# Kernel optimization log

Hardware: AMD Instinct MI355X
Metric: run time of the kernel (lower is better)

## Reference

```python
import math
import jax, jax.numpy as jnp
import numpy as np

N_HEAD = 16


def setup_inputs() -> dict:
    key = jax.random.key(0)
    k1, k2, k3 = jax.random.split(key, 3)
    B, T, D = 2, 2048, 1024
    q = jax.random.normal(k1, (B, T, D), dtype=jnp.float32)
    k = jax.random.normal(k2, (B, T, D), dtype=jnp.float32)
    v = jax.random.normal(k3, (B, T, D), dtype=jnp.float32)
    return {"q": q, "k": k, "v": v}


def _split_heads(x, n_head):
    B, T, D = x.shape
    return x.reshape(B, T, n_head, D // n_head).transpose(0, 2, 1, 3)  # [B,H,T,d]


def _alibi_bias(q_len, k_len, n_head, dtype):
    # bias[t, s] = s - t for s <= t (tril), 0 above diagonal
    rel = jnp.arange(k_len)[None, :] - jnp.arange(q_len)[:, None]
    rel = jnp.tril(rel).astype(dtype)  # [q,k], values <= 0 on lower triangle
    # slopes m_h = 2^(-8*(h+1)/H) via cumprod of constant 2^(-8/H)
    slopes = jnp.cumprod(jnp.full((n_head,), 2.0 ** (-8.0 / n_head), dtype=dtype))
    return rel[None] * slopes[:, None, None]  # [H,q,k]


def reference(q, k, v):
    H = N_HEAD
    qh = _split_heads(q, H)  # [B,H,T,d]
    kh = _split_heads(k, H)
    vh = _split_heads(v, H)
    d = qh.shape[-1]
    attn = jnp.einsum('bhtd,bhsd->bhts', qh, kh) / math.sqrt(d)
    T = qh.shape[2]
    attn = attn + _alibi_bias(T, T, H, attn.dtype)[None]  # broadcast over batch
    causal_mask = jnp.triu(jnp.ones((T, T), dtype=bool), 1)
    attn = jnp.where(causal_mask[None, None], -jnp.inf, attn)
    attn = jax.nn.softmax(attn, axis=-1)
    out = jnp.einsum('bhts,bhsd->bhtd', attn, vh)
    B = out.shape[0]
    return out.transpose(0, 2, 1, 3).reshape(B, T, H * d)
```

## Files before the change

kernel.cpp:

```cpp
#include <hip/hip_runtime.h>
#include <hip/hip_bf16.h>

#define TT 2048
#define DDIM 1024
#define NHEAD 16
#define HD 64
#define QBLK 64
#define KVBLK 64
#define NQT (TT / QBLK)

typedef float f32x4 __attribute__((ext_vector_type(4)));
typedef short bf16x8 __attribute__((ext_vector_type(8)));

__device__ __forceinline__ ushort f2bf(float f) {
    __hip_bfloat16 h = __float2bfloat16(f);
    return *reinterpret_cast<ushort*>(&h);
}

__device__ __forceinline__ void barrier_lgkm_only() {
    asm volatile("s_waitcnt lgkmcnt(0)" ::: "memory");
    __builtin_amdgcn_s_barrier();
}

__global__ __launch_bounds__(256)
void prepass_kernel(const float* __restrict__ kg, const float* __restrict__ vg,
                    ushort* __restrict__ kbf, ushort* __restrict__ vt) {
    __shared__ float vtile[64][65];
    const int tid = threadIdx.x;
    const int kv0 = (int)blockIdx.x * 64;
    const int bh  = (int)blockIdx.y;
    const int b = bh >> 4, h = bh & 15;
    const int row = tid >> 2;
    const int c0  = (tid & 3) * 16;
    const size_t gin = ((size_t)(b * TT + kv0 + row)) * DDIM + h * HD + c0;

    {
        ushort o[16];
        #pragma unroll
        for (int i = 0; i < 4; ++i) {
            float4 a = *(const float4*)(kg + gin + i * 4);
            o[i*4+0]=f2bf(a.x); o[i*4+1]=f2bf(a.y); o[i*4+2]=f2bf(a.z); o[i*4+3]=f2bf(a.w);
        }
        ushort* kout = kbf + ((size_t)bh * TT + kv0 + row) * HD + c0;
        *(bf16x8*)kout       = *(bf16x8*)&o[0];
        *(bf16x8*)(kout + 8) = *(bf16x8*)&o[8];
    }
    #pragma unroll
    for (int i = 0; i < 4; ++i) {
        float4 a = *(const float4*)(vg + gin + i * 4);
        vtile[row][c0 + i*4 + 0] = a.x;
        vtile[row][c0 + i*4 + 1] = a.y;
        vtile[row][c0 + i*4 + 2] = a.z;
        vtile[row][c0 + i*4 + 3] = a.w;
    }
    __syncthreads();
    {
        ushort o[16];
        #pragma unroll
        for (int i = 0; i < 16; ++i) o[i] = f2bf(vtile[c0 + i][row]);
        ushort* vout = vt + ((size_t)bh * HD + row) * TT + kv0 + c0;
        *(bf16x8*)vout       = *(bf16x8*)&o[0];
        *(bf16x8*)(vout + 8) = *(bf16x8*)&o[8];
    }
}

__global__ __launch_bounds__(256, 2)
void attn_main(const float* __restrict__ qg, const ushort* __restrict__ kbf,
               const ushort* __restrict__ vt, float* __restrict__ out) {
    __shared__ __align__(16) ushort lds_k[2][KVBLK * HD];
    __shared__ __align__(16) ushort lds_v[2][HD * KVBLK];
    __shared__ __align__(16) ushort lds_p[4][16 * 64];

    const int tid  = threadIdx.x;
    const int wv   = tid >> 6;
    const int lane = tid & 63;
    const int hi   = lane >> 4;
    const int qr   = lane & 15;

    const int flat = (int)blockIdx.x;
    const int xcd  = flat & 7;
    const int idx  = flat >> 3;
    const int bs   = idx >> 5;
    const int s    = idx & 31;
    const int bh   = xcd * 4 + bs;
    const int qt   = (bs & 1) ? s : (NQT - 1 - s);
    const int b    = bh >> 4;
    const int h    = bh & 15;
    const int q0   = qt * QBLK;

    const float LOG2E  = 1.4426950408889634f;
    const float slope2 = exp2f(-0.5f * (float)(h + 1)) * LOG2E;
    const float sc2    = 0.125f * LOG2E;

    bf16x8 qf[2];
    {
        const float* gq = qg + ((size_t)(b * TT + q0 + wv * 16 + qr)) * DDIM + h * HD + hi * 8;
        #pragma unroll
        for (int ch = 0; ch < 2; ++ch) {
            float4 a0 = *(const float4*)(gq + ch * 32);
            float4 a1 = *(const float4*)(gq + ch * 32 + 4);
            bf16x8 w;
            w[0]=f2bf(a0.x); w[1]=f2bf(a0.y); w[2]=f2bf(a0.z); w[3]=f2bf(a0.w);
            w[4]=f2bf(a1.x); w[5]=f2bf(a1.y); w[6]=f2bf(a1.z); w[7]=f2bf(a1.w);
            qf[ch] = w;
        }
    }

    const ushort* kb = kbf + (size_t)bh * TT * HD;
    const ushort* vb = vt  + (size_t)bh * HD * TT;

    const int srow = tid >> 2;
    const int sci  = tid & 3;

    bf16x8 kr0, kr1, vr0, vr1;
    auto stage_issue = [&](int kv0) {
        const ushort* kp = kb + (size_t)(kv0 + srow) * HD + sci * 8;
        kr0 = *(const bf16x8*)kp;
        kr1 = *(const bf16x8*)(kp + 32);
        const ushort* vp = vb + (size_t)srow * TT + kv0 + sci * 8;
        vr0 = *(const bf16x8*)vp;
        vr1 = *(const bf16x8*)(vp + 32);
    };
    auto stage_write = [&](int nb) {
        const int sw = (srow & 7);
        *(bf16x8*)&lds_k[nb][srow * 64 + ((sci ^ sw) << 3)]       = kr0;
        *(bf16x8*)&lds_k[nb][srow * 64 + (((sci + 4) ^ sw) << 3)] = kr1;
        *(bf16x8*)&lds_v[nb][srow * 64 + ((sci ^ sw) << 3)]       = vr0;
        *(bf16x8*)&lds_v[nb][srow * 64 + (((sci + 4) ^ sw) << 3)] = vr1;
    };

    const int nit = qt + 1;
    stage_issue(q0);
    stage_write(0);

    f32x4 oacc[4] = {};
    float mrun = -INFINITY, lrun = 0.f;
    const int ti = q0 + wv * 16 + qr;

    for (int j = 0; j < nit; ++j) {
        const int buf = j & 1;
        const int kv0 = q0 - j * KVBLK;
        if (j + 1 < nit) stage_issue(kv0 - KVBLK);
        barrier_lgkm_only();

        const bool diag = (j == 0);

        f32x4 sa[4] = {};
        __builtin_amdgcn_s_setprio(1);
        #pragma unroll
        for (int st = 0; st < 4; ++st) {
            if (!diag || st <= wv) {
                const int krow = st * 16 + qr;
                const int sw = (krow & 7);
                bf16x8 k0 = *(const bf16x8*)&lds_k[buf][krow * 64 + ((hi ^ sw) << 3)];
                bf16x8 k1 = *(const bf16x8*)&lds_k[buf][krow * 64 + (((4 + hi) ^ sw) << 3)];
                sa[st] = __builtin_amdgcn_mfma_f32_16x16x32_bf16(k0, qf[0], sa[st], 0, 0, 0);
                sa[st] = __builtin_amdgcn_mfma_f32_16x16x32_bf16(k1, qf[1], sa[st], 0, 0, 0);
            }
        }
        __builtin_amdgcn_s_setprio(0);

        const float relb = (float)(kv0 - ti + hi * 4);
        float xv[16];
        float tm = -INFINITY;
        #pragma unroll
        for (int st = 0; st < 4; ++st)
            #pragma unroll
            for (int rr = 0; rr < 4; ++rr) {
                const float rel = relb + (float)(st * 16 + rr);
                float v = fmaf(sa[st][rr], sc2, rel * slope2);
                if (diag) v = (rel <= 0.f) ? v : -INFINITY;
                xv[st * 4 + rr] = v;
                tm = fmaxf(tm, v);
            }
        tm = fmaxf(tm, __shfl_xor(tm, 16));
        tm = fmaxf(tm, __shfl_xor(tm, 32));
        if (!__all(tm <= mrun + 8.f)) {
            const float mnew = fmaxf(mrun, tm);
            const float fsc  = exp2f(mrun - mnew);
            mrun = mnew;
            lrun *= fsc;
            float fo[4];
            #pragma unroll
            for (int rr = 0; rr < 4; ++rr) fo[rr] = __shfl(fsc, hi * 4 + rr);
            #pragma unroll
            for (int dt = 0; dt < 4; ++dt)
                #pragma unroll
                for (int rr = 0; rr < 4; ++rr) oacc[dt][rr] *= fo[rr];
        }
        float psum = 0.f;
        #pragma unroll
        for (int i = 0; i < 16; ++i) { xv[i] = exp2f(xv[i] - mrun); psum += xv[i]; }
        lrun += psum;

        #pragma unroll
        for (int st = 0; st < 4; ++st) {
            ushort4 w;
            w.x = f2bf(xv[st * 4 + 0]); w.y = f2bf(xv[st * 4 + 1]);
            w.z = f2bf(xv[st * 4 + 2]); w.w = f2bf(xv[st * 4 + 3]);
            const int slot8 = (st << 1) | (hi >> 1);
            *(ushort4*)&lds_p[wv][qr * 64 + ((slot8 ^ (qr & 7)) << 3) + ((hi & 1) << 2)] = w;
        }

        __builtin_amdgcn_s_setprio(1);
        #pragma unroll
        for (int ks = 0; ks < 2; ++ks) {
            if (!diag || wv >= 2 || ks == 0) {
                bf16x8 pa = *(const bf16x8*)&lds_p[wv][qr * 64 + ((((ks << 2) | hi) ^ (qr & 7)) << 3)];
                #pragma unroll
                for (int dt = 0; dt < 4; ++dt) {
                    const int dv = dt * 16 + qr;
                    bf16x8 vbf = *(const bf16x8*)&lds_v[buf][dv * 64 + ((((ks << 2) + hi) ^ (dv & 7)) << 3)];
                    oacc[dt] = __builtin_amdgcn_mfma_f32_16x16x32_bf16(pa, vbf, oacc[dt], 0, 0, 0);
                }
            }
        }
        __builtin_amdgcn_s_setprio(0);

        if (j + 1 < nit) stage_write(buf ^ 1);
    }

    {
        float lr = lrun;
        lr += __shfl_xor(lr, 16);
        lr += __shfl_xor(lr, 32);
        const float linv = 1.0f / lr;
        #pragma unroll
        for (int rr = 0; rr < 4; ++rr) {
            const float inv = __shfl(linv, hi * 4 + rr);
            float* go = out + ((size_t)(b * TT + q0 + wv * 16 + hi * 4 + rr)) * DDIM + h * HD;
            #pragma unroll
            for (int dt = 0; dt < 4; ++dt)
                go[dt * 16 + qr] = oacc[dt][rr] * inv;
        }
    }
}

#define VST 72
__global__ __launch_bounds__(256, 2)
void alibi_attn_fallback(const float* __restrict__ qg,
                         const float* __restrict__ kg,
                         const float* __restrict__ vg,
                         float* __restrict__ out) {
    __shared__ __align__(16) ushort lds_k[KVBLK * HD];
    __shared__ __align__(16) ushort lds_vt[HD * VST];
    __shared__ __align__(16) ushort lds_p[4][16 * 64];

    const int tid  = threadIdx.x;
    const int wv   = tid >> 6;
    const int lane = tid & 63;
    const int hi   = lane >> 4;
    const int qr   = lane & 15;

    const int flat = (int)blockIdx.x;
    const int xcd  = flat & 7;
    const int idx  = flat >> 3;
    const int bh   = xcd * 4 + (idx >> 5);
    const int qt   = NQT - 1 - (idx & 31);
    const int b    = bh >> 4;
    const int h    = bh & 15;
    const int q0   = qt * QBLK;

    const float LOG2E  = 1.4426950408889634f;
    const float slope2 = exp2f(-0.5f * (float)(h + 1)) * LOG2E;
    const float sc2    = 0.125f * LOG2E;

    const size_t bhbase = (size_t)(b * TT) * DDIM + (size_t)(h * HD);

    bf16x8 qf[2];
    {
        const float* gq = qg + bhbase + (size_t)(q0 + wv * 16 + qr) * DDIM + hi * 8;
        #pragma unroll
        for (int ch = 0; ch < 2; ++ch) {
            float4 a0 = *(const float4*)(gq + ch * 32);
            float4 a1 = *(const float4*)(gq + ch * 32 + 4);
            bf16x8 w;
            w[0]=f2bf(a0.x); w[1]=f2bf(a0.y); w[2]=f2bf(a0.z); w[3]=f2bf(a0.w);
            w[4]=f2bf(a1.x); w[5]=f2bf(a1.y); w[6]=f2bf(a1.z); w[7]=f2bf(a1.w);
            qf[ch] = w;
        }
    }

    const int krow = tid >> 3;
    const int kcg  = tid & 7;
    const int vdv  = tid & 63;
    const int vkc  = tid >> 6;

    float ka[2][8], va[2][8];
    auto issue_loads = [&](int kv0) {
        const float* kp0 = kg + bhbase + (size_t)(kv0 + krow) * DDIM + kcg * 8;
        const float* kp1 = kp0 + (size_t)32 * DDIM;
        *(float4*)&ka[0][0] = *(const float4*)kp0; *(float4*)&ka[0][4] = *(const float4*)(kp0 + 4);
        *(float4*)&ka[1][0] = *(const float4*)kp1; *(float4*)&ka[1][4] = *(const float4*)(kp1 + 4);
        const float* vp0 = vg + bhbase + (size_t)(kv0 + vkc * 8) * DDIM + vdv;
        const float* vp1 = vp0 + (size_t)32 * DDIM;
        #pragma unroll
        for (int jj = 0; jj < 8; ++jj) {
            va[0][jj] = vp0[(size_t)jj * DDIM];
            va[1][jj] = vp1[(size_t)jj * DDIM];
        }
    };
    auto write_stage = [&]() {
        #pragma unroll
        for (int s2 = 0; s2 < 2; ++s2) {
            bf16x8 w;
            #pragma unroll
            for (int e = 0; e < 8; ++e) w[e] = f2bf(ka[s2][e]);
            const int row = krow + s2 * 32;
            *(bf16x8*)&lds_k[row * 64 + ((kcg ^ (row & 7)) << 3)] = w;
            bf16x8 u;
            #pragma unroll
            for (int e = 0; e < 8; ++e) u[e] = f2bf(va[s2][e]);
            const int kc = vkc + s2 * 4;
            *(bf16x8*)&lds_vt[vdv * VST + ((kc ^ ((vdv >> 3) & 7)) << 3)] = u;
        }
    };

    const int nit = qt + 1;
    issue_loads(q0);
    write_stage();

    f32x4 oacc[4] = {};
    float mrun = -INFINITY, lrun = 0.f;

    for (int j = 0; j < nit; ++j) {
        const int kv0 = (qt - j) * KVBLK;
        if (j + 1 < nit) issue_loads(kv0 - KVBLK);
        __syncthreads();

        const bool diag = (j == 0);

        f32x4 s_acc[4] = {};
        __builtin_amdgcn_s_setprio(1);
        #pragma unroll
        for (int st = 0; st < 4; ++st) {
            if (!diag || st <= wv) {
                const int kvrow = st * 16 + qr;
                #pragma unroll
                for (int ch = 0; ch < 2; ++ch) {
                    bf16x8 kf = *(const bf16x8*)&lds_k[kvrow * 64 + ((((ch << 2) + hi) ^ (kvrow & 7)) << 3)];
                    s_acc[st] = __builtin_amdgcn_mfma_f32_16x16x32_bf16(kf, qf[ch], s_acc[st], 0, 0, 0);
                }
            }
        }
        __builtin_amdgcn_s_setprio(0);

        const int ti = q0 + wv * 16 + qr;
        float xv[16];
        float tm = -INFINITY;
        {
            const float relb = (float)(kv0 - ti);
            #pragma unroll
            for (int st = 0; st < 4; ++st)
                #pragma unroll
                for (int rr = 0; rr < 4; ++rr) {
                    const float rel = relb + (float)(st * 16 + hi * 4 + rr);
                    float v = s_acc[st][rr] * sc2 + rel * slope2;
                    if (diag) v = (rel <= 0.f) ? v : -INFINITY;
                    xv[st * 4 + rr] = v;
                    tm = fmaxf(tm, v);
                }
        }
        tm = fmaxf(tm, __shfl_xor(tm, 16));
        tm = fmaxf(tm, __shfl_xor(tm, 32));
        if (!__all(tm <= mrun + 8.f)) {
            const float mnew = fmaxf(mrun, tm);
            const float fsc  = exp2f(mrun - mnew);
            mrun = mnew;
            lrun *= fsc;
            float fo[4];
            #pragma unroll
            for (int rr = 0; rr < 4; ++rr) fo[rr] = __shfl(fsc, hi * 4 + rr);
            #pragma unroll
            for (int dt = 0; dt < 4; ++dt)
                #pragma unroll
                for (int rr = 0; rr < 4; ++rr) oacc[dt][rr] *= fo[rr];
        }
        float psum = 0.f;
        #pragma unroll
        for (int i = 0; i < 16; ++i) { xv[i] = exp2f(xv[i] - mrun); psum += xv[i]; }
        lrun += psum;

        #pragma unroll
        for (int st = 0; st < 4; ++st) {
            ushort4 w;
            w.x = f2bf(xv[st * 4 + 0]); w.y = f2bf(xv[st * 4 + 1]);
            w.z = f2bf(xv[st * 4 + 2]); w.w = f2bf(xv[st * 4 + 3]);
            const int slot8 = (st << 1) | (hi >> 1);
            *(ushort4*)&lds_p[wv][qr * 64 + ((slot8 ^ (qr & 7)) << 3) + ((hi & 1) << 2)] = w;
        }

        __builtin_amdgcn_s_setprio(1);
        #pragma unroll
        for (int ks = 0; ks < 2; ++ks) {
            if (!diag || wv >= 2 || ks == 0) {
                bf16x8 pa = *(const bf16x8*)&lds_p[wv][qr * 64 + ((((ks << 2) | hi) ^ (qr & 7)) << 3)];
                #pragma unroll
                for (int dt = 0; dt < 4; ++dt) {
                    const int dv = dt * 16 + qr;
                    bf16x8 vbf = *(const bf16x8*)&lds_vt[dv * VST + ((((ks << 2) + hi) ^ ((dv >> 3) & 7)) << 3)];
                    oacc[dt] = __builtin_amdgcn_mfma_f32_16x16x32_bf16(pa, vbf, oacc[dt], 0, 0, 0);
                }
            }
        }
        __builtin_amdgcn_s_setprio(0);

        if (j + 1 < nit) {
            __syncthreads();
            write_stage();
        }
    }

    {
        float lr = lrun;
        lr += __shfl_xor(lr, 16);
        lr += __shfl_xor(lr, 32);
        const float linv = 1.0f / lr;
        #pragma unroll
        for (int rr = 0; rr < 4; ++rr) {
            const float inv = __shfl(linv, hi * 4 + rr);
            float* go = out + bhbase + (size_t)(q0 + wv * 16 + hi * 4 + rr) * DDIM;
            #pragma unroll
            for (int dt = 0; dt < 4; ++dt)
                go[dt * 16 + qr] = oacc[dt][rr] * inv;
        }
    }
}

extern "C" void kernel_launch(void* const* d_in, const int* in_sizes, int n_in,
                              void* d_out, int out_size, void* d_ws, size_t ws_size,
                              hipStream_t stream) {
    (void)in_sizes; (void)n_in; (void)out_size;
    const float* q = (const float*)d_in[0];
    const float* k = (const float*)d_in[1];
    const float* v = (const float*)d_in[2];
    float* o = (float*)d_out;

    const size_t elems = (size_t)2 * NHEAD * TT * HD;
    const size_t need  = 2 * elems * sizeof(ushort);
    if (ws_size >= need) {
        ushort* kbf = (ushort*)d_ws;
        ushort* vt  = kbf + elems;
        prepass_kernel<<<dim3(32, 32), 256, 0, stream>>>(k, v, kbf, vt);
        attn_main<<<dim3(1024), 256, 0, stream>>>(q, kbf, vt, o);
    } else {
        alibi_attn_fallback<<<dim3(1024), 256, 0, stream>>>(q, k, v, o);
    }
}
```

Baseline: 65.34 us.

## Split heavy causal query tiles across two blocks and merge with a combine kernel

Query tiles 16-31 have their KV range cut in half, and each half runs in its own block, giving 1536 blocks instead of 1024. This evens out the causal workload imbalance. Split blocks write unnormalized partial outputs plus running max/sum to workspace, and a new combine kernel merges them. It also precomputes per-element ALiBi offsets and moves the cross-lane max shuffle inside the rescale branch. This adds a third launch and extra global traffic for the partials, and the fallback path for small workspace is removed.

After: 68.48 us. +4.8%, slower.

```diff
diff --git a/kernel.cpp b/kernel.cpp
--- a/kernel.cpp
+++ b/kernel.cpp
@@ -65,8 +65,9 @@
 }
 
 __global__ __launch_bounds__(256, 2)
-void attn_main(const float* __restrict__ qg, const ushort* __restrict__ kbf,
-               const ushort* __restrict__ vt, float* __restrict__ out) {
+void attn_split(const float* __restrict__ qg, const ushort* __restrict__ kbf,
+                const ushort* __restrict__ vtt, float* __restrict__ po,
+                float* __restrict__ ml, float* __restrict__ out) {
     __shared__ __align__(16) ushort lds_k[2][KVBLK * HD];
     __shared__ __align__(16) ushort lds_v[2][HD * KVBLK];
     __shared__ __align__(16) ushort lds_p[4][16 * 64];
@@ -79,18 +80,27 @@
 
     const int flat = (int)blockIdx.x;
     const int xcd  = flat & 7;
-    const int idx  = flat >> 3;
-    const int bs   = idx >> 5;
-    const int s    = idx & 31;
-    const int bh   = xcd * 4 + bs;
-    const int qt   = (bs & 1) ? s : (NQT - 1 - s);
-    const int b    = bh >> 4;
-    const int h    = bh & 15;
-    const int q0   = qt * QBLK;
+    const int i2   = flat >> 3;
+    const int bh   = xcd * 4 + (i2 & 3);
+    const int id   = i2 >> 2;
+    int qt, lo, thi, part = 0;
+    bool hasdiag, heavy;
+    if (id < 16)      { qt = 16 + id;        const int n = qt + 1; lo = n >> 1; thi = n;      hasdiag = true;  heavy = true; part = 0; }
+    else if (id < 32) { qt = 31 - (id - 16); const int n = qt + 1; lo = 0;      thi = n >> 1; hasdiag = false; heavy = true; part = 1; }
+    else              { qt = id - 32;        lo = 0; thi = qt + 1; hasdiag = true; heavy = false; }
+    const int nt = thi - lo;
+    const int b  = bh >> 4;
+    const int h  = bh & 15;
+    const int q0 = qt * QBLK;
 
     const float LOG2E  = 1.4426950408889634f;
     const float slope2 = exp2f(-0.5f * (float)(h + 1)) * LOG2E;
     const float sc2    = 0.125f * LOG2E;
+    float c2[16];
+    #pragma unroll
+    for (int st = 0; st < 4; ++st)
+        #pragma unroll
+        for (int rr = 0; rr < 4; ++rr) c2[st * 4 + rr] = (float)(st * 16 + rr) * slope2;
 
     bf16x8 qf[2];
     {
@@ -107,7 +117,7 @@
     }
 
     const ushort* kb = kbf + (size_t)bh * TT * HD;
-    const ushort* vb = vt  + (size_t)bh * HD * TT;
+    const ushort* vb = vtt + (size_t)bh * HD * TT;
 
     const int srow = tid >> 2;
     const int sci  = tid & 3;
@@ -129,6 +139,233 @@
         *(bf16x8*)&lds_v[nb][srow * 64 + (((sci + 4) ^ sw) << 3)] = vr1;
     };
 
+    stage_issue((thi - 1) * KVBLK);
+    stage_write(0);
+
+    f32x4 oacc[4] = {};
+    float mrun = -INFINITY, lrun = 0.f;
+    const int ti = q0 + wv * 16 + qr;
+
+    for (int j = 0; j < nt; ++j) {
+        const int buf = j & 1;
+        const int t   = thi - 1 - j;
+        const int kv0 = t * KVBLK;
+        if (j + 1 < nt) stage_issue((t - 1) * KVBLK);
+        barrier_lgkm_only();
+
+        const bool diag = (j == 0) && hasdiag;
+
+        f32x4 sa[4] = {};
+        __builtin_amdgcn_s_setprio(1);
+        #pragma unroll
+        for (int st = 0; st < 4; ++st) {
+            if (!diag || st <= wv) {
+                const int krow = st * 16 + qr;
+                const int sw = (krow & 7);
+                bf16x8 k0 = *(const bf16x8*)&lds_k[buf][krow * 64 + ((hi ^ sw) << 3)];
+                bf16x8 k1 = *(const bf16x8*)&lds_k[buf][krow * 64 + (((4 + hi) ^ sw) << 3)];
+                sa[st] = __builtin_amdgcn_mfma_f32_16x16x32_bf16(k0, qf[0], sa[st], 0, 0, 0);
+                sa[st] = __builtin_amdgcn_mfma_f32_16x16x32_bf16(k1, qf[1], sa[st], 0, 0, 0);
+            }
+        }
+        __builtin_amdgcn_s_setprio(0);
+
+        const float relb  = (float)(kv0 - ti + hi * 4);
+        const float relb2 = relb * slope2;
+        float xv[16];
+        float tm = -INFINITY;
+        #pragma unroll
+        for (int st = 0; st < 4; ++st)
+            #pragma unroll
+            for (int rr = 0; rr < 4; ++rr) {
+                float v = fmaf(sa[st][rr], sc2, relb2 + c2[st * 4 + rr]);
+                if (diag) {
+                    const float rel = relb + (float)(st * 16 + rr);
+                    v = (rel <= 0.f) ? v : -INFINITY;
+                }
+                xv[st * 4 + rr] = v;
+                tm = fmaxf(tm, v);
+            }
+        if (!__all(tm <= mrun + 8.f)) {
+            tm = fmaxf(tm, __shfl_xor(tm, 16));
+            tm = fmaxf(tm, __shfl_xor(tm, 32));
+            const float mnew = fmaxf(mrun, tm);
+            const float fsc  = exp2f(mrun - mnew);
+            mrun = mnew;
+            lrun *= fsc;
+            float fo[4];
+            #pragma unroll
+            for (int rr = 0; rr < 4; ++rr) fo[rr] = __shfl(fsc, hi * 4 + rr);
+            #pragma unroll
+            for (int dt = 0; dt < 4; ++dt)
+                #pragma unroll
+                for (int rr = 0; rr < 4; ++rr) oacc[dt][rr] *= fo[rr];
+        }
+        float psum = 0.f;
+        #pragma unroll
+        for (int i = 0; i < 16; ++i) { xv[i] = exp2f(xv[i] - mrun); psum += xv[i]; }
+        lrun += psum;
+
+        #pragma unroll
+        for (int st = 0; st < 4; ++st) {
+            ushort4 w;
+            w.x = f2bf(xv[st * 4 + 0]); w.y = f2bf(xv[st * 4 + 1]);
+            w.z = f2bf(xv[st * 4 + 2]); w.w = f2bf(xv[st * 4 + 3]);
+            const int slot8 = (st << 1) | (hi >> 1);
+            *(ushort4*)&lds_p[wv][qr * 64 + ((slot8 ^ (qr & 7)) << 3) + ((hi & 1) << 2)] = w;
+        }
+
+        __builtin_amdgcn_s_setprio(1);
+        #pragma unroll
+        for (int ks = 0; ks < 2; ++ks) {
+            if (!diag || wv >= 2 || ks == 0) {
+                bf16x8 pa = *(const bf16x8*)&lds_p[wv][qr * 64 + ((((ks << 2) | hi) ^ (qr & 7)) << 3)];
+                #pragma unroll
+                for (int dt = 0; dt < 4; ++dt) {
+                    const int dv = dt * 16 + qr;
+                    bf16x8 vbf = *(const bf16x8*)&lds_v[buf][dv * 64 + ((((ks << 2) + hi) ^ (dv & 7)) << 3)];
+                    oacc[dt] = __builtin_amdgcn_mfma_f32_16x16x32_bf16(pa, vbf, oacc[dt], 0, 0, 0);
+                }
+            }
+        }
+        __builtin_amdgcn_s_setprio(0);
+
+        if (j + 1 < nt) stage_write(buf ^ 1);
+    }
+
+    float lr = lrun;
+    lr += __shfl_xor(lr, 16);
+    lr += __shfl_xor(lr, 32);
+    if (!heavy) {
+        const float linv = 1.0f / lr;
+        #pragma unroll
+        for (int rr = 0; rr < 4; ++rr) {
+            const float inv = __shfl(linv, hi * 4 + rr);
+            float* go = out + ((size_t)(b * TT + q0 + wv * 16 + hi * 4 + rr)) * DDIM + h * HD;
+            #pragma unroll
+            for (int dt = 0; dt < 4; ++dt)
+                go[dt * 16 + qr] = oacc[dt][rr] * inv;
+        }
+    } else {
+        float* pbase = po + ((size_t)((part * 32 + bh) * 16 + (qt - 16))) * 4096;
+        #pragma unroll
+        for (int rr = 0; rr < 4; ++rr) {
+            const int row = wv * 16 + hi * 4 + rr;
+            #pragma unroll
+            for (int dt = 0; dt < 4; ++dt)
+                pbase[row * 64 + dt * 16 + qr] = oacc[dt][rr];
+        }
+        if (hi == 0) {
+            float* mlb = ml + ((size_t)((part * 32 + bh) * 16 + (qt - 16))) * 128 + (wv * 16 + qr) * 2;
+            mlb[0] = mrun;
+            mlb[1] = lr;
+        }
+    }
+}
+
+__global__ __launch_bounds__(256)
+void combine_kernel(const float* __restrict__ po, const float* __restrict__ ml,
+                    float* __restrict__ out) {
+    const int blk = (int)blockIdx.x;
+    const int bh  = blk >> 4;
+    const int q16 = blk & 15;
+    const int qt  = 16 + q16;
+    const int b = bh >> 4, h = bh & 15;
+    const int tid = threadIdx.x;
+    const int row = tid >> 2;
+    const int c0  = (tid & 3) * 16;
+
+    const float* ml0 = ml + ((size_t)((0 * 32 + bh) * 16 + q16)) * 128 + row * 2;
+    const float* ml1 = ml + ((size_t)((1 * 32 + bh) * 16 + q16)) * 128 + row * 2;
+    const float m0 = ml0[0], l0 = ml0[1];
+    const float m1 = ml1[0], l1 = ml1[1];
+    const float m  = fmaxf(m0, m1);
+    const float a0 = exp2f(m0 - m);
+    const float a1 = exp2f(m1 - m);
+    const float linv = 1.0f / fmaf(l0, a0, l1 * a1);
+    const float s0 = a0 * linv, s1 = a1 * linv;
+
+    const float* p0 = po + ((size_t)((0 * 32 + bh) * 16 + q16) * 64 + row) * 64 + c0;
+    const float* p1 = po + ((size_t)((1 * 32 + bh) * 16 + q16) * 64 + row) * 64 + c0;
+    float* go = out + ((size_t)(b * TT + qt * 64 + row)) * DDIM + h * HD + c0;
+    #pragma unroll
+    for (int i = 0; i < 4; ++i) {
+        float4 x0 = *(const float4*)(p0 + i * 4);
+        float4 x1 = *(const float4*)(p1 + i * 4);
+        float4 r;
+        r.x = x0.x * s0 + x1.x * s1;
+        r.y = x0.y * s0 + x1.y * s1;
+        r.z = x0.z * s0 + x1.z * s1;
+        r.w = x0.w * s0 + x1.w * s1;
+        *(float4*)(go + i * 4) = r;
+    }
+}
+
+__global__ __launch_bounds__(256, 2)
+void attn_main(const float* __restrict__ qg, const ushort* __restrict__ kbf,
+               const ushort* __restrict__ vt, float* __restrict__ out) {
+    __shared__ __align__(16) ushort lds_k[2][KVBLK * HD];
+    __shared__ __align__(16) ushort lds_v[2][HD * KVBLK];
+    __shared__ __align__(16) ushort lds_p[4][16 * 64];
+
+    const int tid  = threadIdx.x;
+    const int wv   = tid >> 6;
+    const int lane = tid & 63;
+    const int hi   = lane >> 4;
+    const int qr   = lane & 15;
+
+    const int flat = (int)blockIdx.x;
+    const int xcd  = flat & 7;
+    const int idx  = flat >> 3;
+    const int bs   = idx >> 5;
+    const int s    = idx & 31;
+    const int bh   = xcd * 4 + bs;
+    const int qt   = (bs & 1) ? s : (NQT - 1 - s);
+    const int b    = bh >> 4;
+    const int h    = bh & 15;
+    const int q0   = qt * QBLK;
+
+    const float LOG2E  = 1.4426950408889634f;
+    const float slope2 = exp2f(-0.5f * (float)(h + 1)) * LOG2E;
+    const float sc2    = 0.125f * LOG2E;
+
+    bf16x8 qf[2];
+    {
+        const float* gq = qg + ((size_t)(b * TT + q0 + wv * 16 + qr)) * DDIM + h * HD + hi * 8;
+        #pragma unroll
+        for (int ch = 0; ch < 2; ++ch) {
+            float4 a0 = *(const float4*)(gq + ch * 32);
+            float4 a1 = *(const float4*)(gq + ch * 32 + 4);
+            bf16x8 w;
+            w[0]=f2bf(a0.x); w[1]=f2bf(a0.y); w[2]=f2bf(a0.z); w[3]=f2bf(a0.w);
+            w[4]=f2bf(a1.x); w[5]=f2bf(a1.y); w[6]=f2bf(a1.z); w[7]=f2bf(a1.w);
+            qf[ch] = w;
+        }
+    }
+
+    const ushort* kb = kbf + (size_t)bh * TT * HD;
+    const ushort* vb = vt  + (size_t)bh * HD * TT;
+
+    const int srow = tid >> 2;
+    const int sci  = tid & 3;
+
+    bf16x8 kr0, kr1, vr0, vr1;
+    auto stage_issue = [&](int kv0) {
+        const ushort* kp = kb + (size_t)(kv0 + srow) * HD + sci * 8;
+        kr0 = *(const bf16x8*)kp;
+        kr1 = *(const bf16x8*)(kp + 32);
+        const ushort* vp = vb + (size_t)srow * TT + kv0 + sci * 8;
+        vr0 = *(const bf16x8*)vp;
+        vr1 = *(const bf16x8*)(vp + 32);
+    };
+    auto stage_write = [&](int nb) {
+        const int sw = (srow & 7);
+        *(bf16x8*)&lds_k[nb][srow * 64 + ((sci ^ sw) << 3)]       = kr0;
+        *(bf16x8*)&lds_k[nb][srow * 64 + (((sci + 4) ^ sw) << 3)] = kr1;
+        *(bf16x8*)&lds_v[nb][srow * 64 + ((sci ^ sw) << 3)]       = vr0;
+        *(bf16x8*)&lds_v[nb][srow * 64 + (((sci + 4) ^ sw) << 3)] = vr1;
+    };
+
     const int nit = qt + 1;
     stage_issue(q0);
     stage_write(0);
@@ -236,197 +473,6 @@
     }
 }
 
-#define VST 72
-__global__ __launch_bounds__(256, 2)
-void alibi_attn_fallback(const float* __restrict__ qg,
-                         const float* __restrict__ kg,
-                         const float* __restrict__ vg,
-                         float* __restrict__ out) {
-    __shared__ __align__(16) ushort lds_k[KVBLK * HD];
-    __shared__ __align__(16) ushort lds_vt[HD * VST];
-    __shared__ __align__(16) ushort lds_p[4][16 * 64];
-
-    const int tid  = threadIdx.x;
-    const int wv   = tid >> 6;
-    const int lane = tid & 63;
-    const int hi   = lane >> 4;
-    const int qr   = lane & 15;
-
-    const int flat = (int)blockIdx.x;
-    const int xcd  = flat & 7;
-    const int idx  = flat >> 3;
-    const int bh   = xcd * 4 + (idx >> 5);
-    const int qt   = NQT - 1 - (idx & 31);
-    const int b    = bh >> 4;
-    const int h    = bh & 15;
-    const int q0   = qt * QBLK;
-
-    const float LOG2E  = 1.4426950408889634f;
-    const float slope2 = exp2f(-0.5f * (float)(h + 1)) * LOG2E;
-    const float sc2    = 0.125f * LOG2E;
-
-    const size_t bhbase = (size_t)(b * TT) * DDIM + (size_t)(h * HD);
-
-    bf16x8 qf[2];
-    {
-        const float* gq = qg + bhbase + (size_t)(q0 + wv * 16 + qr) * DDIM + hi * 8;
-        #pragma unroll
-        for (int ch = 0; ch < 2; ++ch) {
-            float4 a0 = *(const float4*)(gq + ch * 32);
-            float4 a1 = *(const float4*)(gq + ch * 32 + 4);
-            bf16x8 w;
-            w[0]=f2bf(a0.x); w[1]=f2bf(a0.y); w[2]=f2bf(a0.z); w[3]=f2bf(a0.w);
-            w[4]=f2bf(a1.x); w[5]=f2bf(a1.y); w[6]=f2bf(a1.z); w[7]=f2bf(a1.w);
-            qf[ch] = w;
-        }
-    }
-
-    const int krow = tid >> 3;
-    const int kcg  = tid & 7;
-    const int vdv  = tid & 63;
-    const int vkc  = tid >> 6;
-
-    float ka[2][8], va[2][8];
-    auto issue_loads = [&](int kv0) {
-        const float* kp0 = kg + bhbase + (size_t)(kv0 + krow) * DDIM + kcg * 8;
-        const float* kp1 = kp0 + (size_t)32 * DDIM;
-        *(float4*)&ka[0][0] = *(const float4*)kp0; *(float4*)&ka[0][4] = *(const float4*)(kp0 + 4);
-        *(float4*)&ka[1][0] = *(const float4*)kp1; *(float4*)&ka[1][4] = *(const float4*)(kp1 + 4);
-        const float* vp0 = vg + bhbase + (size_t)(kv0 + vkc * 8) * DDIM + vdv;
-        const float* vp1 = vp0 + (size_t)32 * DDIM;
-        #pragma unroll
-        for (int jj = 0; jj < 8; ++jj) {
-            va[0][jj] = vp0[(size_t)jj * DDIM];
-            va[1][jj] = vp1[(size_t)jj * DDIM];
-        }
-    };
-    auto write_stage = [&]() {
-        #pragma unroll
-        for (int s2 = 0; s2 < 2; ++s2) {
-            bf16x8 w;
-            #pragma unroll
-            for (int e = 0; e < 8; ++e) w[e] = f2bf(ka[s2][e]);
-            const int row = krow + s2 * 32;
-            *(bf16x8*)&lds_k[row * 64 + ((kcg ^ (row & 7)) << 3)] = w;
-            bf16x8 u;
-            #pragma unroll
-            for (int e = 0; e < 8; ++e) u[e] = f2bf(va[s2][e]);
-            const int kc = vkc + s2 * 4;
-            *(bf16x8*)&lds_vt[vdv * VST + ((kc ^ ((vdv >> 3) & 7)) << 3)] = u;
-        }
-    };
-
-    const int nit = qt + 1;
-    issue_loads(q0);
-    write_stage();
-
-    f32x4 oacc[4] = {};
-    float mrun = -INFINITY, lrun = 0.f;
-
-    for (int j = 0; j < nit; ++j) {
-        const int kv0 = (qt - j) * KVBLK;
-        if (j + 1 < nit) issue_loads(kv0 - KVBLK);
-        __syncthreads();
-
-        const bool diag = (j == 0);
-
-        f32x4 s_acc[4] = {};
-        __builtin_amdgcn_s_setprio(1);
-        #pragma unroll
-        for (int st = 0; st < 4; ++st) {
-            if (!diag || st <= wv) {
-                const int kvrow = st * 16 + qr;
-                #pragma unroll
-                for (int ch = 0; ch < 2; ++ch) {
-                    bf16x8 kf = *(const bf16x8*)&lds_k[kvrow * 64 + ((((ch << 2) + hi) ^ (kvrow & 7)) << 3)];
-                    s_acc[st] = __builtin_amdgcn_mfma_f32_16x16x32_bf16(kf, qf[ch], s_acc[st], 0, 0, 0);
-                }
-            }
-        }
-        __builtin_amdgcn_s_setprio(0);
-
-        const int ti = q0 + wv * 16 + qr;
-        float xv[16];
-        float tm = -INFINITY;
-        {
-            const float relb = (float)(kv0 - ti);
-            #pragma unroll
-            for (int st = 0; st < 4; ++st)
-                #pragma unroll
-                for (int rr = 0; rr < 4; ++rr) {
-                    const float rel = relb + (float)(st * 16 + hi * 4 + rr);
-                    float v = s_acc[st][rr] * sc2 + rel * slope2;
-                    if (diag) v = (rel <= 0.f) ? v : -INFINITY;
-                    xv[st * 4 + rr] = v;
-                    tm = fmaxf(tm, v);
-                }
-        }
-        tm = fmaxf(tm, __shfl_xor(tm, 16));
-        tm = fmaxf(tm, __shfl_xor(tm, 32));
-        if (!__all(tm <= mrun + 8.f)) {
-            const float mnew = fmaxf(mrun, tm);
-            const float fsc  = exp2f(mrun - mnew);
-            mrun = mnew;
-            lrun *= fsc;
-            float fo[4];
-            #pragma unroll
-            for (int rr = 0; rr < 4; ++rr) fo[rr] = __shfl(fsc, hi * 4 + rr);
-            #pragma unroll
-            for (int dt = 0; dt < 4; ++dt)
-                #pragma unroll
-                for (int rr = 0; rr < 4; ++rr) oacc[dt][rr] *= fo[rr];
-        }
-        float psum = 0.f;
-        #pragma unroll
-        for (int i = 0; i < 16; ++i) { xv[i] = exp2f(xv[i] - mrun); psum += xv[i]; }
-        lrun += psum;
-
-        #pragma unroll
-        for (int st = 0; st < 4; ++st) {
-            ushort4 w;
-            w.x = f2bf(xv[st * 4 + 0]); w.y = f2bf(xv[st * 4 + 1]);
-            w.z = f2bf(xv[st * 4 + 2]); w.w = f2bf(xv[st * 4 + 3]);
-            const int slot8 = (st << 1) | (hi >> 1);
-            *(ushort4*)&lds_p[wv][qr * 64 + ((slot8 ^ (qr & 7)) << 3) + ((hi & 1) << 2)] = w;
-        }
-
-        __builtin_amdgcn_s_setprio(1);
-        #pragma unroll
-        for (int ks = 0; ks < 2; ++ks) {
-            if (!diag || wv >= 2 || ks == 0) {
-                bf16x8 pa = *(const bf16x8*)&lds_p[wv][qr * 64 + ((((ks << 2) | hi) ^ (qr & 7)) << 3)];
-                #pragma unroll
-                for (int dt = 0; dt < 4; ++dt) {
-                    const int dv = dt * 16 + qr;
-                    bf16x8 vbf = *(const bf16x8*)&lds_vt[dv * VST + ((((ks << 2) + hi) ^ ((dv >> 3) & 7)) << 3)];
-                    oacc[dt] = __builtin_amdgcn_mfma_f32_16x16x32_bf16(pa, vbf, oacc[dt], 0, 0, 0);
-                }
-            }
-        }
-        __builtin_amdgcn_s_setprio(0);
-
-        if (j + 1 < nit) {
-            __syncthreads();
-            write_stage();
-        }
-    }
-
-    {
-        float lr = lrun;
-        lr += __shfl_xor(lr, 16);
-        lr += __shfl_xor(lr, 32);
-        const float linv = 1.0f / lr;
-        #pragma unroll
-        for (int rr = 0; rr < 4; ++rr) {
-            const float inv = __shfl(linv, hi * 4 + rr);
-            float* go = out + bhbase + (size_t)(q0 + wv * 16 + hi * 4 + rr) * DDIM;
-            #pragma unroll
-            for (int dt = 0; dt < 4; ++dt)
-                go[dt * 16 + qr] = oacc[dt][rr] * inv;
-        }
-    }
-}
-
 extern "C" void kernel_launch(void* const* d_in, const int* in_sizes, int n_in,
                               void* d_out, int out_size, void* d_ws, size_t ws_size,
                               hipStream_t stream) {
@@ -436,14 +482,22 @@
     const float* v = (const float*)d_in[2];
     float* o = (float*)d_out;
 
-    const size_t elems = (size_t)2 * NHEAD * TT * HD;
-    const size_t need  = 2 * elems * sizeof(ushort);
-    if (ws_size >= need) {
+    const size_t elems   = (size_t)2 * NHEAD * TT * HD;
+    const size_t kv_b    = 2 * elems * sizeof(ushort);
+    const size_t po_b    = (size_t)2 * 32 * 16 * 64 * 64 * sizeof(float);
+    const size_t ml_b    = (size_t)2 * 32 * 16 * 64 * 2 * sizeof(float);
+    if (ws_size >= kv_b + po_b + ml_b) {
         ushort* kbf = (ushort*)d_ws;
-        ushort* vt  = kbf + elems;
-        prepass_kernel<<<dim3(32, 32), 256, 0, stream>>>(k, v, kbf, vt);
-        attn_main<<<dim3(1024), 256, 0, stream>>>(q, kbf, vt, o);
-    } else {
-        alibi_attn_fallback<<<dim3(1024), 256, 0, stream>>>(q, k, v, o);
-    }
-}
+        ushort* vtt = kbf + elems;
+        float*  po  = (float*)((char*)d_ws + kv_b);
+        float*  ml  = po + (size_t)2 * 32 * 16 * 64 * 64;
+        prepass_kernel<<<dim3(32, 32), 256, 0, stream>>>(k, v, kbf, vtt);
+        attn_split<<<dim3(1536), 256, 0, stream>>>(q, kbf, vtt, po, ml, o);
+        combine_kernel<<<dim3(512), 256, 0, stream>>>(po, ml, o);
+    } else if (ws_size >= kv_b) {
+        ushort* kbf = (ushort*)d_ws;
+        ushort* vtt = kbf + elems;
+        prepass_kernel<<<dim3(32, 32), 256, 0, stream>>>(k, v, kbf, vtt);
+        attn_main<<<dim3(1024), 256, 0, stream>>>(q, kbf, vtt, o);
+    }
+}
```

## Load V fragments directly from global into registers, bypassing LDS staging

Applied to the files above, without the earlier changes.

V tiles are no longer staged through a double-buffered LDS buffer. Each wave now loads its V MFMA operand fragments straight from the transposed global V into registers at the start of every KV iteration. This removes LDS writes and reads for V and halves LDS use, which may allow higher occupancy, but each wave now issues redundant, uncoalesced-ish global loads whose latency is only partly hidden before the PV MFMAs. It also precomputes the per-column ALiBi offsets and moves the cross-lane max reduction inside the rescale branch.

Result: slower. 107.6 us (+64.6%).

```diff
diff --git a/kernel.cpp b/kernel.cpp
--- a/kernel.cpp
+++ b/kernel.cpp
@@ -68,7 +68,6 @@
 void attn_main(const float* __restrict__ qg, const ushort* __restrict__ kbf,
                const ushort* __restrict__ vt, float* __restrict__ out) {
     __shared__ __align__(16) ushort lds_k[2][KVBLK * HD];
-    __shared__ __align__(16) ushort lds_v[2][HD * KVBLK];
     __shared__ __align__(16) ushort lds_p[4][16 * 64];
 
     const int tid  = threadIdx.x;
@@ -91,6 +90,11 @@
     const float LOG2E  = 1.4426950408889634f;
     const float slope2 = exp2f(-0.5f * (float)(h + 1)) * LOG2E;
     const float sc2    = 0.125f * LOG2E;
+    float c2[16];
+    #pragma unroll
+    for (int st = 0; st < 4; ++st)
+        #pragma unroll
+        for (int rr = 0; rr < 4; ++rr) c2[st * 4 + rr] = (float)(st * 16 + rr) * slope2;
 
     bf16x8 qf[2];
     {
@@ -112,21 +116,16 @@
     const int srow = tid >> 2;
     const int sci  = tid & 3;
 
-    bf16x8 kr0, kr1, vr0, vr1;
+    bf16x8 kr0, kr1;
     auto stage_issue = [&](int kv0) {
         const ushort* kp = kb + (size_t)(kv0 + srow) * HD + sci * 8;
         kr0 = *(const bf16x8*)kp;
         kr1 = *(const bf16x8*)(kp + 32);
-        const ushort* vp = vb + (size_t)srow * TT + kv0 + sci * 8;
-        vr0 = *(const bf16x8*)vp;
-        vr1 = *(const bf16x8*)(vp + 32);
     };
     auto stage_write = [&](int nb) {
         const int sw = (srow & 7);
         *(bf16x8*)&lds_k[nb][srow * 64 + ((sci ^ sw) << 3)]       = kr0;
         *(bf16x8*)&lds_k[nb][srow * 64 + (((sci + 4) ^ sw) << 3)] = kr1;
-        *(bf16x8*)&lds_v[nb][srow * 64 + ((sci ^ sw) << 3)]       = vr0;
-        *(bf16x8*)&lds_v[nb][srow * 64 + (((sci + 4) ^ sw) << 3)] = vr1;
     };
 
     const int nit = qt + 1;
@@ -140,10 +139,17 @@
     for (int j = 0; j < nit; ++j) {
         const int buf = j & 1;
         const int kv0 = q0 - j * KVBLK;
+        const bool diag = (j == 0);
+
+        bf16x8 vfr[2][4];
+        #pragma unroll
+        for (int ks = 0; ks < 2; ++ks)
+            #pragma unroll
+            for (int dt = 0; dt < 4; ++dt)
+                vfr[ks][dt] = *(const bf16x8*)(vb + (size_t)(dt * 16 + qr) * TT + kv0 + ks * 32 + hi * 8);
+
         if (j + 1 < nit) stage_issue(kv0 - KVBLK);
         barrier_lgkm_only();
-
-        const bool diag = (j == 0);
 
         f32x4 sa[4] = {};
         __builtin_amdgcn_s_setprio(1);
@@ -160,22 +166,25 @@
         }
         __builtin_amdgcn_s_setprio(0);
 
-        const float relb = (float)(kv0 - ti + hi * 4);
+        const float relb  = (float)(kv0 - ti + hi * 4);
+        const float relb2 = relb * slope2;
         float xv[16];
         float tm = -INFINITY;
         #pragma unroll
         for (int st = 0; st < 4; ++st)
             #pragma unroll
             for (int rr = 0; rr < 4; ++rr) {
-                const float rel = relb + (float)(st * 16 + rr);
-                float v = fmaf(sa[st][rr], sc2, rel * slope2);
-                if (diag) v = (rel <= 0.f) ? v : -INFINITY;
+                float v = fmaf(sa[st][rr], sc2, relb2 + c2[st * 4 + rr]);
+                if (diag) {
+                    const float rel = relb + (float)(st * 16 + rr);
+                    v = (rel <= 0.f) ? v : -INFINITY;
+                }
                 xv[st * 4 + rr] = v;
                 tm = fmaxf(tm, v);
             }
-        tm = fmaxf(tm, __shfl_xor(tm, 16));
-        tm = fmaxf(tm, __shfl_xor(tm, 32));
         if (!__all(tm <= mrun + 8.f)) {
+            tm = fmaxf(tm, __shfl_xor(tm, 16));
+            tm = fmaxf(tm, __shfl_xor(tm, 32));
             const float mnew = fmaxf(mrun, tm);
             const float fsc  = exp2f(mrun - mnew);
             mrun = mnew;
@@ -208,11 +217,8 @@
             if (!diag || wv >= 2 || ks == 0) {
                 bf16x8 pa = *(const bf16x8*)&lds_p[wv][qr * 64 + ((((ks << 2) | hi) ^ (qr & 7)) << 3)];
                 #pragma unroll
-                for (int dt = 0; dt < 4; ++dt) {
-                    const int dv = dt * 16 + qr;
-                    bf16x8 vbf = *(const bf16x8*)&lds_v[buf][dv * 64 + ((((ks << 2) + hi) ^ (dv & 7)) << 3)];
-                    oacc[dt] = __builtin_amdgcn_mfma_f32_16x16x32_bf16(pa, vbf, oacc[dt], 0, 0, 0);
-                }
+                for (int dt = 0; dt < 4; ++dt)
+                    oacc[dt] = __builtin_amdgcn_mfma_f32_16x16x32_bf16(pa, vfr[ks][dt], oacc[dt], 0, 0, 0);
             }
         }
         __builtin_amdgcn_s_setprio(0);
@@ -437,12 +443,12 @@
     float* o = (float*)d_out;
 
     const size_t elems = (size_t)2 * NHEAD * TT * HD;
-    const size_t need  = 2 * elems * sizeof(ushort);
-    if (ws_size >= need) {
+    const size_t kv_b  = 2 * elems * sizeof(ushort);
+    if (ws_size >= kv_b) {
         ushort* kbf = (ushort*)d_ws;
-        ushort* vt  = kbf + elems;
-        prepass_kernel<<<dim3(32, 32), 256, 0, stream>>>(k, v, kbf, vt);
-        attn_main<<<dim3(1024), 256, 0, stream>>>(q, kbf, vt, o);
+        ushort* vtt = kbf + elems;
+        prepass_kernel<<<dim3(32, 32), 256, 0, stream>>>(k, v, kbf, vtt);
+        attn_main<<<dim3(1024), 256, 0, stream>>>(q, kbf, vtt, o);
     } else {
         alibi_attn_fallback<<<dim3(1024), 256, 0, stream>>>(q, k, v, o);
     }
```
